# Optimization experiments

Hardware: AMD Instinct MI355X
Metric: run time of the kernel (lower is better)

The kernel has to match this reference:

```python
import jax, jax.numpy as jnp
import numpy as np

EMBED_SIZE = 768
HEAD_SIZE = 64
B, T = 4, 2048


def setup_inputs() -> dict:
    key = jax.random.key(0)
    kx, kk, kq, kv = jax.random.split(key, 4)
    x = jax.random.normal(kx, (B, T, EMBED_SIZE), dtype=jnp.float32)
    # torch Linear(E, H, bias=False): weight [H, E]; stored here as [E, H] for x @ W
    s = 1.0 / np.sqrt(EMBED_SIZE)
    Wk = jax.random.uniform(kk, (EMBED_SIZE, HEAD_SIZE), jnp.float32, -s, s)
    Wq = jax.random.uniform(kq, (EMBED_SIZE, HEAD_SIZE), jnp.float32, -s, s)
    Wv = jax.random.uniform(kv, (EMBED_SIZE, HEAD_SIZE), jnp.float32, -s, s)
    return {"x": x, "Wk": Wk, "Wq": Wq, "Wv": Wv}


def reference(x, Wk, Wq, Wv):
    Bx, Tx, E = x.shape
    k = x @ Wk  # [B, T, H]
    q = x @ Wq
    v = x @ Wv
    w = jnp.einsum("bth,bsh->bts", q, k)  # [B, T, T]
    causal = jnp.tril(jnp.ones((Tx, Tx), dtype=bool))
    # Faithful to source: mask to -inf FIRST, then scale by sqrt(embed_size)
    w = jnp.where(causal, w, -jnp.inf)
    w = w / jnp.sqrt(jnp.asarray(E, dtype=x.dtype))
    w = jax.nn.softmax(w, axis=-1)
    # dropout: eval mode / identity for the correctness baseline
    return jnp.einsum("bts,bsh->bth", w, v)
```

## Files before the change

kernel.cpp:

```cpp
#include <hip/hip_runtime.h>
#include <hip/hip_bf16.h>


typedef __attribute__((ext_vector_type(8))) short short8;
typedef __attribute__((ext_vector_type(4))) float f32x4;

#define SPLIT_KB 4
#define MAX_SP 8

__device__ __forceinline__ unsigned short f2bf(float f) {
    union { float f; unsigned u; } v; v.f = f;
    unsigned r = v.u + 0x7fffu + ((v.u >> 16) & 1u);
    return (unsigned short)(r >> 16);
}

__global__ __launch_bounds__(256) void proj_kernel(const float* __restrict__ x,
                                                   const float* __restrict__ Wk,
                                                   const float* __restrict__ Wq,
                                                   const float* __restrict__ Wv,
                                                   unsigned short* __restrict__ qws,
                                                   unsigned short* __restrict__ kws,
                                                   unsigned short* __restrict__ vT) {
    __shared__ unsigned short xs[32 * 72];
    __shared__ unsigned short wsm[64 * 72];
    const float CSCALE = 1.4426950408889634f / 27.712812921102035f;
    int tid = threadIdx.x;
    int lane = tid & 63, wave = tid >> 6;
    int quad = lane >> 4, l16 = lane & 15;
    int row0 = blockIdx.x * 32;
    int my = blockIdx.y;
    const float* W = (my == 0) ? Wq : (my == 1) ? Wk : Wv;

    int xrow = tid >> 3, xcb = (tid & 7) * 8;
    int wn = tid & 63, wk0 = (tid >> 6) * 16;

    f32x4 acc[2];
    acc[0] = (f32x4)(0.f); acc[1] = (f32x4)(0.f);

    for (int kc = 0; kc < 12; ++kc) {
        __syncthreads();
        {
            const float* src = x + (size_t)(row0 + xrow) * 768 + kc * 64 + xcb;
            float4 f0 = *(const float4*)(src);
            float4 f1 = *(const float4*)(src + 4);
            short8 pk;
            pk[0] = (short)f2bf(f0.x); pk[1] = (short)f2bf(f0.y);
            pk[2] = (short)f2bf(f0.z); pk[3] = (short)f2bf(f0.w);
            pk[4] = (short)f2bf(f1.x); pk[5] = (short)f2bf(f1.y);
            pk[6] = (short)f2bf(f1.z); pk[7] = (short)f2bf(f1.w);
            *(short8*)&xs[xrow * 72 + xcb] = pk;
        }
        {
            float wv[16];
            for (int i = 0; i < 16; ++i)
                wv[i] = W[(size_t)(kc * 64 + wk0 + i) * 64 + wn];
            if (my == 0)
                for (int i = 0; i < 16; ++i) wv[i] *= CSCALE;
            short8 p0, p1;
            for (int i = 0; i < 8; ++i) { p0[i] = (short)f2bf(wv[i]); p1[i] = (short)f2bf(wv[8 + i]); }
            *(short8*)&wsm[wn * 72 + wk0] = p0;
            *(short8*)&wsm[wn * 72 + wk0 + 8] = p1;
        }
        __syncthreads();
        for (int kh = 0; kh < 2; ++kh) {
            int kk = kh * 32 + quad * 8;
            short8 bfr = *(const short8*)&wsm[(wave * 16 + l16) * 72 + kk];
            for (int mt = 0; mt < 2; ++mt) {
                short8 a = *(const short8*)&xs[(mt * 16 + l16) * 72 + kk];
                acc[mt] = __builtin_amdgcn_mfma_f32_16x16x32_bf16(a, bfr, acc[mt], 0, 0, 0);
            }
        }
    }
    __syncthreads();
    int n = wave * 16 + l16;
    if (my != 2) {
        unsigned short* dst = (my == 0) ? qws : kws;
        for (int mt = 0; mt < 2; ++mt)
            for (int j = 0; j < 4; ++j) {
                int rloc = mt * 16 + quad * 4 + j;
                dst[(size_t)(row0 + rloc) * 64 + n] = f2bf(acc[mt][j]);
            }
    } else {
        for (int mt = 0; mt < 2; ++mt)
            for (int j = 0; j < 4; ++j) {
                int rloc = mt * 16 + quad * 4 + j;
                wsm[n * 40 + rloc] = f2bf(acc[mt][j]);
            }
        __syncthreads();
        int bidx = row0 >> 11, t0 = row0 & 2047;
        int c = tid >> 2, rb = (tid & 3) * 8;
        *(short8*)&vT[((size_t)(bidx * 64 + c)) * 2048 + t0 + rb] =
            *(const short8*)&wsm[c * 40 + rb];
    }
}

__global__ __launch_bounds__(128) void attn_split(const unsigned short* __restrict__ qws,
                                                  const unsigned short* __restrict__ kws,
                                                  const unsigned short* __restrict__ vT,
                                                  float* __restrict__ po,
                                                  float* __restrict__ pl,
                                                  float* __restrict__ out) {
    int bx = blockIdx.x, b = blockIdx.y, sp = blockIdx.z;
    int kbmax = (bx >> 1) + 1;
    int nsp = (kbmax + SPLIT_KB - 1) / SPLIT_KB;
    if (sp >= nsp) return;
    int kb_lo = sp * SPLIT_KB;
    int kb_hi = min(kb_lo + SPLIT_KB, kbmax);

    __shared__ unsigned short qs[32 * 72];
    __shared__ unsigned short ks[64 * 72];
    __shared__ unsigned short vs[64 * 72];
    __shared__ unsigned short ps[2][16 * 72];
    int tid = threadIdx.x;
    int lane = tid & 63, wave = tid >> 6;
    int quad = lane >> 4, l16 = lane & 15;
    int q0 = bx * 32;
    size_t qbase = ((size_t)b * 2048 + q0) * 64;
    for (int i = 0; i < 2; ++i) {
        int e = tid + 128 * i;
        int r = e >> 3, hb = (e & 7) * 8;
        *(short8*)&qs[r * 72 + hb] = *(const short8*)&qws[qbase + r * 64 + hb];
    }
    __syncthreads();
    short8 aq[2];
    for (int kh = 0; kh < 2; ++kh)
        aq[kh] = *(const short8*)&qs[(wave * 16 + l16) * 72 + kh * 32 + quad * 8];

    f32x4 o_acc[4];
    for (int nt = 0; nt < 4; ++nt) o_acc[nt] = (f32x4)(0.f);
    float l_run[4];
    int row_g[4];
    for (int j = 0; j < 4; ++j) {
        l_run[j] = 0.f;
        row_g[j] = q0 + wave * 16 + quad * 4 + j;
    }

    for (int kb = kb_lo; kb < kb_hi; ++kb) {
        __syncthreads();
        size_t kvbase = ((size_t)b * 2048 + kb * 64) * 64;
        for (int i = 0; i < 4; ++i) {
            int e = tid + 128 * i;
            int r = e >> 3, hb = (e & 7) * 8;
            *(short8*)&ks[r * 72 + hb] = *(const short8*)&kws[kvbase + r * 64 + hb];
        }
        for (int i = 0; i < 4; ++i) {
            int e = tid + 128 * i;
            int h = e >> 3, kyb = (e & 7) * 8;
            *(short8*)&vs[h * 72 + kyb] =
                *(const short8*)&vT[((size_t)b * 64 + h) * 2048 + kb * 64 + kyb];
        }
        __syncthreads();
        f32x4 s[4];
        for (int nt = 0; nt < 4; ++nt) s[nt] = (f32x4)(0.f);
        for (int kh = 0; kh < 2; ++kh)
            for (int nt = 0; nt < 4; ++nt) {
                short8 bk = *(const short8*)&ks[(nt * 16 + l16) * 72 + kh * 32 + quad * 8];
                s[nt] = __builtin_amdgcn_mfma_f32_16x16x32_bf16(aq[kh], bk, s[nt], 0, 0, 0);
            }
        if (kb == kbmax - 1) {
            for (int nt = 0; nt < 4; ++nt) {
                int key = kb * 64 + nt * 16 + l16;
                for (int j = 0; j < 4; ++j)
                    if (key > row_g[j]) s[nt][j] = -1e30f;
            }
        }
        for (int nt = 0; nt < 4; ++nt)
            for (int j = 0; j < 4; ++j) {
                float p = exp2f(s[nt][j]);
                l_run[j] += p;
                ps[wave][(quad * 4 + j) * 72 + nt * 16 + l16] = f2bf(p);
            }
        for (int kh = 0; kh < 2; ++kh) {
            short8 ap = *(const short8*)&ps[wave][l16 * 72 + kh * 32 + quad * 8];
            for (int nt = 0; nt < 4; ++nt) {
                short8 bv = *(const short8*)&vs[(nt * 16 + l16) * 72 + kh * 32 + quad * 8];
                o_acc[nt] = __builtin_amdgcn_mfma_f32_16x16x32_bf16(ap, bv, o_acc[nt], 0, 0, 0);
            }
        }
    }
    for (int off = 1; off < 16; off <<= 1)
        for (int j = 0; j < 4; ++j)
            l_run[j] += __shfl_xor(l_run[j], off, 16);

    if (nsp == 1) {
        for (int nt = 0; nt < 4; ++nt)
            for (int j = 0; j < 4; ++j)
                out[((size_t)b * 2048 + row_g[j]) * 64 + nt * 16 + l16] =
                    o_acc[nt][j] / l_run[j];
        return;
    }
    int sbase = ((b * 64 + bx) * MAX_SP + sp) * 32;
    for (int nt = 0; nt < 4; ++nt)
        for (int j = 0; j < 4; ++j) {
            int r = wave * 16 + quad * 4 + j;
            po[(size_t)(sbase + r) * 64 + nt * 16 + l16] = o_acc[nt][j];
        }
    if (l16 == 0) {
        for (int j = 0; j < 4; ++j) {
            int r = wave * 16 + quad * 4 + j;
            pl[sbase + r] = l_run[j];
        }
    }
}

__global__ __launch_bounds__(256) void reduce_kernel(const float* __restrict__ po,
                                                     const float* __restrict__ pl,
                                                     float* __restrict__ out) {
    int tid = threadIdx.x;
    int lane = tid & 63, wave = tid >> 6;
    int g = blockIdx.x * 4 + wave;
    int b = g >> 11, t = g & 2047;
    int bx = t >> 5, r = t & 31;
    int kbmax = (bx >> 1) + 1;
    int nsp = (kbmax + SPLIT_KB - 1) / SPLIT_KB;
    if (nsp == 1) return;
    int base = ((b * 64 + bx) * MAX_SP) * 32 + r;
    float acc = 0.f, lsum = 0.f;
    for (int sp = 0; sp < nsp; ++sp) {
        acc += po[(size_t)(base + sp * 32) * 64 + lane];
        lsum += pl[base + sp * 32];
    }
    out[(size_t)g * 64 + lane] = acc / lsum;
}

extern "C" void kernel_launch(void* const* d_in, const int* in_sizes, int n_in,
                              void* d_out, int out_size, void* d_ws, size_t ws_size,
                              hipStream_t stream) {
    const float* x  = (const float*)d_in[0];
    const float* Wk = (const float*)d_in[1];
    const float* Wq = (const float*)d_in[2];
    const float* Wv = (const float*)d_in[3];
    float* out = (float*)d_out;
    char* w = (char*)d_ws;
    unsigned short* qws = (unsigned short*)w;
    unsigned short* kws = (unsigned short*)(w + 1048576);
    unsigned short* vT  = (unsigned short*)(w + 2097152);
    float* po = (float*)(w + 3145728);
    float* pl = (float*)(w + 19922944);
    proj_kernel<<<dim3(256, 3), 256, 0, stream>>>(x, Wk, Wq, Wv, qws, kws, vT);
    attn_split<<<dim3(64, 4, MAX_SP), 128, 0, stream>>>(qws, kws, vT, po, pl, out);
    reduce_kernel<<<2048, 256, 0, stream>>>(po, pl, out);
}
```

Before: 101.6 us.

## Halve projection row tile and read weights directly into MFMA fragments

```diff
diff --git a/kernel.cpp b/kernel.cpp
--- a/kernel.cpp
+++ b/kernel.cpp
@@ -21,76 +21,63 @@
                                                    unsigned short* __restrict__ qws,
                                                    unsigned short* __restrict__ kws,
                                                    unsigned short* __restrict__ vT) {
-    __shared__ unsigned short xs[32 * 72];
-    __shared__ unsigned short wsm[64 * 72];
+    __shared__ unsigned short xs[16 * 72];
+    __shared__ unsigned short vsm[64 * 24];
     const float CSCALE = 1.4426950408889634f / 27.712812921102035f;
     int tid = threadIdx.x;
     int lane = tid & 63, wave = tid >> 6;
     int quad = lane >> 4, l16 = lane & 15;
-    int row0 = blockIdx.x * 32;
+    int row0 = blockIdx.x * 16;
     int my = blockIdx.y;
     const float* W = (my == 0) ? Wq : (my == 1) ? Wk : Wv;
 
-    int xrow = tid >> 3, xcb = (tid & 7) * 8;
-    int wn = tid & 63, wk0 = (tid >> 6) * 16;
-
-    f32x4 acc[2];
-    acc[0] = (f32x4)(0.f); acc[1] = (f32x4)(0.f);
+    int xrow = tid >> 4, xcb = (tid & 15) * 4;
+
+    f32x4 acc = (f32x4)(0.f);
 
     for (int kc = 0; kc < 12; ++kc) {
         __syncthreads();
         {
             const float* src = x + (size_t)(row0 + xrow) * 768 + kc * 64 + xcb;
             float4 f0 = *(const float4*)(src);
-            float4 f1 = *(const float4*)(src + 4);
-            short8 pk;
-            pk[0] = (short)f2bf(f0.x); pk[1] = (short)f2bf(f0.y);
-            pk[2] = (short)f2bf(f0.z); pk[3] = (short)f2bf(f0.w);
-            pk[4] = (short)f2bf(f1.x); pk[5] = (short)f2bf(f1.y);
-            pk[6] = (short)f2bf(f1.z); pk[7] = (short)f2bf(f1.w);
-            *(short8*)&xs[xrow * 72 + xcb] = pk;
-        }
-        {
-            float wv[16];
-            for (int i = 0; i < 16; ++i)
-                wv[i] = W[(size_t)(kc * 64 + wk0 + i) * 64 + wn];
-            if (my == 0)
-                for (int i = 0; i < 16; ++i) wv[i] *= CSCALE;
-            short8 p0, p1;
-            for (int i = 0; i < 8; ++i) { p0[i] = (short)f2bf(wv[i]); p1[i] = (short)f2bf(wv[8 + i]); }
-            *(short8*)&wsm[wn * 72 + wk0] = p0;
-            *(short8*)&wsm[wn * 72 + wk0 + 8] = p1;
+            unsigned short* d = &xs[xrow * 72 + xcb];
+            d[0] = f2bf(f0.x); d[1] = f2bf(f0.y);
+            d[2] = f2bf(f0.z); d[3] = f2bf(f0.w);
         }
         __syncthreads();
         for (int kh = 0; kh < 2; ++kh) {
-            int kk = kh * 32 + quad * 8;
-            short8 bfr = *(const short8*)&wsm[(wave * 16 + l16) * 72 + kk];
-            for (int mt = 0; mt < 2; ++mt) {
-                short8 a = *(const short8*)&xs[(mt * 16 + l16) * 72 + kk];
-                acc[mt] = __builtin_amdgcn_mfma_f32_16x16x32_bf16(a, bfr, acc[mt], 0, 0, 0);
-            }
-        }
-    }
-    __syncthreads();
+            short8 a = *(const short8*)&xs[l16 * 72 + kh * 32 + quad * 8];
+            const float* Wp = W + (size_t)(kc * 64 + kh * 32 + quad * 8) * 64
+                                + wave * 16 + l16;
+            short8 bfr;
+            #pragma unroll
+            for (int j = 0; j < 8; ++j) {
+                float wv = Wp[j * 64];
+                if (my == 0) wv *= CSCALE;
+                bfr[j] = (short)f2bf(wv);
+            }
+            acc = __builtin_amdgcn_mfma_f32_16x16x32_bf16(a, bfr, acc, 0, 0, 0);
+        }
+    }
     int n = wave * 16 + l16;
     if (my != 2) {
         unsigned short* dst = (my == 0) ? qws : kws;
-        for (int mt = 0; mt < 2; ++mt)
-            for (int j = 0; j < 4; ++j) {
-                int rloc = mt * 16 + quad * 4 + j;
-                dst[(size_t)(row0 + rloc) * 64 + n] = f2bf(acc[mt][j]);
-            }
+        for (int j = 0; j < 4; ++j) {
+            int rloc = quad * 4 + j;
+            dst[(size_t)(row0 + rloc) * 64 + n] = f2bf(acc[j]);
+        }
     } else {
-        for (int mt = 0; mt < 2; ++mt)
-            for (int j = 0; j < 4; ++j) {
-                int rloc = mt * 16 + quad * 4 + j;
-                wsm[n * 40 + rloc] = f2bf(acc[mt][j]);
-            }
-        __syncthreads();
-        int bidx = row0 >> 11, t0 = row0 & 2047;
-        int c = tid >> 2, rb = (tid & 3) * 8;
-        *(short8*)&vT[((size_t)(bidx * 64 + c)) * 2048 + t0 + rb] =
-            *(const short8*)&wsm[c * 40 + rb];
+        for (int j = 0; j < 4; ++j) {
+            int rloc = quad * 4 + j;
+            vsm[n * 24 + rloc] = f2bf(acc[j]);
+        }
+        __syncthreads();
+        if (tid < 128) {
+            int bidx = row0 >> 11, t0 = row0 & 2047;
+            int c = tid >> 1, rb = (tid & 1) * 8;
+            *(short8*)&vT[((size_t)(bidx * 64 + c)) * 2048 + t0 + rb] =
+                *(const short8*)&vsm[c * 24 + rb];
+        }
     }
 }
 
@@ -128,12 +115,10 @@
 
     f32x4 o_acc[4];
     for (int nt = 0; nt < 4; ++nt) o_acc[nt] = (f32x4)(0.f);
-    float l_run[4];
+    float l_run[4] = {0.f, 0.f, 0.f, 0.f};
     int row_g[4];
-    for (int j = 0; j < 4; ++j) {
-        l_run[j] = 0.f;
+    for (int j = 0; j < 4; ++j)
         row_g[j] = q0 + wave * 16 + quad * 4 + j;
-    }
 
     for (int kb = kb_lo; kb < kb_hi; ++kb) {
         __syncthreads();
@@ -237,7 +222,7 @@
     unsigned short* vT  = (unsigned short*)(w + 2097152);
     float* po = (float*)(w + 3145728);
     float* pl = (float*)(w + 19922944);
-    proj_kernel<<<dim3(256, 3), 256, 0, stream>>>(x, Wk, Wq, Wv, qws, kws, vT);
+    proj_kernel<<<dim3(512, 3), 256, 0, stream>>>(x, Wk, Wq, Wv, qws, kws, vT);
     attn_split<<<dim3(64, 4, MAX_SP), 128, 0, stream>>>(qws, kws, vT, po, pl, out);
     reduce_kernel<<<2048, 256, 0, stream>>>(po, pl, out);
 }
```

Result: slower. 109.4 us (+7.6%).

## Fuse projection, attention and reduction into one cooperative persistent kernel

Applied to the files above, without the earlier changes.

```diff
diff --git a/kernel.cpp b/kernel.cpp
--- a/kernel.cpp
+++ b/kernel.cpp
@@ -1,5 +1,8 @@
 #include <hip/hip_runtime.h>
 #include <hip/hip_bf16.h>
+#include <hip/hip_cooperative_groups.h>
+
+namespace cg = cooperative_groups;
 
 
 typedef __attribute__((ext_vector_type(8))) short short8;
@@ -12,6 +15,195 @@
     union { float f; unsigned u; } v; v.f = f;
     unsigned r = v.u + 0x7fffu + ((v.u >> 16) & 1u);
     return (unsigned short)(r >> 16);
+}
+
+__global__ __launch_bounds__(128, 2) void mega_kernel(
+        const float* __restrict__ x,  const float* __restrict__ Wk,
+        const float* __restrict__ Wq, const float* __restrict__ Wv,
+        unsigned short* __restrict__ qws, unsigned short* __restrict__ kws,
+        unsigned short* __restrict__ vT,  float* __restrict__ po,
+        float* __restrict__ pl, float* __restrict__ out) {
+    cg::grid_group grid = cg::this_grid();
+    __shared__ __align__(16) char smem[27648];
+    const float CSCALE = 1.4426950408889634f / 27.712812921102035f;
+    int tid = threadIdx.x;
+    int lane = tid & 63, wave = tid >> 6;
+    int quad = lane >> 4, l16 = lane & 15;
+
+    {
+        unsigned short* xs  = (unsigned short*)smem;
+        unsigned short* wsm = xs + 16 * 72;
+        unsigned short* vsm = wsm + 64 * 72;
+        int xrow = tid >> 3, xcb = (tid & 7) * 8;
+        int wn = tid & 63, wk0 = (tid >> 6) * 32;
+        for (int it = blockIdx.x; it < 1536; it += 512) {
+            int my = it >> 9;
+            int row0 = (it & 511) * 16;
+            const float* W = (my == 0) ? Wq : (my == 1) ? Wk : Wv;
+            f32x4 acc[2];
+            acc[0] = (f32x4)(0.f); acc[1] = (f32x4)(0.f);
+            for (int kc = 0; kc < 12; ++kc) {
+                __syncthreads();
+                {
+                    const float* src = x + (size_t)(row0 + xrow) * 768 + kc * 64 + xcb;
+                    float4 f0 = *(const float4*)(src);
+                    float4 f1 = *(const float4*)(src + 4);
+                    short8 pk;
+                    pk[0] = (short)f2bf(f0.x); pk[1] = (short)f2bf(f0.y);
+                    pk[2] = (short)f2bf(f0.z); pk[3] = (short)f2bf(f0.w);
+                    pk[4] = (short)f2bf(f1.x); pk[5] = (short)f2bf(f1.y);
+                    pk[6] = (short)f2bf(f1.z); pk[7] = (short)f2bf(f1.w);
+                    *(short8*)&xs[xrow * 72 + xcb] = pk;
+                }
+                for (int g = 0; g < 4; ++g) {
+                    float wv[8]; short8 p;
+                    #pragma unroll
+                    for (int i = 0; i < 8; ++i)
+                        wv[i] = W[(size_t)(kc * 64 + wk0 + g * 8 + i) * 64 + wn];
+                    if (my == 0)
+                        for (int i = 0; i < 8; ++i) wv[i] *= CSCALE;
+                    for (int i = 0; i < 8; ++i) p[i] = (short)f2bf(wv[i]);
+                    *(short8*)&wsm[wn * 72 + wk0 + g * 8] = p;
+                }
+                __syncthreads();
+                for (int kh = 0; kh < 2; ++kh) {
+                    int kk = kh * 32 + quad * 8;
+                    short8 a = *(const short8*)&xs[l16 * 72 + kk];
+                    for (int nt = 0; nt < 2; ++nt) {
+                        short8 bfr = *(const short8*)&wsm[(wave * 32 + nt * 16 + l16) * 72 + kk];
+                        acc[nt] = __builtin_amdgcn_mfma_f32_16x16x32_bf16(a, bfr, acc[nt], 0, 0, 0);
+                    }
+                }
+            }
+            if (my != 2) {
+                unsigned short* dst = (my == 0) ? qws : kws;
+                for (int nt = 0; nt < 2; ++nt)
+                    for (int j = 0; j < 4; ++j)
+                        dst[(size_t)(row0 + quad * 4 + j) * 64 + wave * 32 + nt * 16 + l16] =
+                            f2bf(acc[nt][j]);
+            } else {
+                for (int nt = 0; nt < 2; ++nt)
+                    for (int j = 0; j < 4; ++j)
+                        vsm[(wave * 32 + nt * 16 + l16) * 24 + quad * 4 + j] = f2bf(acc[nt][j]);
+                __syncthreads();
+                int bidx = row0 >> 11, t0 = row0 & 2047;
+                int c = tid >> 1, rb = (tid & 1) * 8;
+                *(short8*)&vT[((size_t)(bidx * 64 + c)) * 2048 + t0 + rb] =
+                    *(const short8*)&vsm[c * 24 + rb];
+            }
+        }
+    }
+    grid.sync();
+    {
+        unsigned short* qs = (unsigned short*)smem;
+        unsigned short* ks = qs + 32 * 72;
+        unsigned short* vs = ks + 64 * 72;
+        unsigned short* ps = vs + 64 * 72;
+        for (int i2 = blockIdx.x; i2 < 2048; i2 += 512) {
+            int bx = i2 & 63, b = (i2 >> 6) & 3, sp = i2 >> 8;
+            int kbmax = (bx >> 1) + 1;
+            int nsp = (kbmax + SPLIT_KB - 1) / SPLIT_KB;
+            if (sp >= nsp) continue;
+            int kb_lo = sp * SPLIT_KB;
+            int kb_hi = min(kb_lo + SPLIT_KB, kbmax);
+            int q0 = bx * 32;
+            size_t qbase = ((size_t)b * 2048 + q0) * 64;
+            for (int i = 0; i < 2; ++i) {
+                int e = tid + 128 * i;
+                int r = e >> 3, hb = (e & 7) * 8;
+                *(short8*)&qs[r * 72 + hb] = *(const short8*)&qws[qbase + r * 64 + hb];
+            }
+            __syncthreads();
+            short8 aq[2];
+            for (int kh = 0; kh < 2; ++kh)
+                aq[kh] = *(const short8*)&qs[(wave * 16 + l16) * 72 + kh * 32 + quad * 8];
+            f32x4 o_acc[4];
+            for (int nt = 0; nt < 4; ++nt) o_acc[nt] = (f32x4)(0.f);
+            float l_run[4] = {0.f, 0.f, 0.f, 0.f};
+            int row_g[4];
+            for (int j = 0; j < 4; ++j)
+                row_g[j] = q0 + wave * 16 + quad * 4 + j;
+            for (int kb = kb_lo; kb < kb_hi; ++kb) {
+                __syncthreads();
+                size_t kvbase = ((size_t)b * 2048 + kb * 64) * 64;
+                for (int i = 0; i < 4; ++i) {
+                    int e = tid + 128 * i;
+                    int r = e >> 3, hb = (e & 7) * 8;
+                    *(short8*)&ks[r * 72 + hb] = *(const short8*)&kws[kvbase + r * 64 + hb];
+                }
+                for (int i = 0; i < 4; ++i) {
+                    int e = tid + 128 * i;
+                    int h = e >> 3, kyb = (e & 7) * 8;
+                    *(short8*)&vs[h * 72 + kyb] =
+                        *(const short8*)&vT[((size_t)b * 64 + h) * 2048 + kb * 64 + kyb];
+                }
+                __syncthreads();
+                f32x4 s[4];
+                for (int nt = 0; nt < 4; ++nt) s[nt] = (f32x4)(0.f);
+                for (int kh = 0; kh < 2; ++kh)
+                    for (int nt = 0; nt < 4; ++nt) {
+                        short8 bk = *(const short8*)&ks[(nt * 16 + l16) * 72 + kh * 32 + quad * 8];
+                        s[nt] = __builtin_amdgcn_mfma_f32_16x16x32_bf16(aq[kh], bk, s[nt], 0, 0, 0);
+                    }
+                if (kb == kbmax - 1) {
+                    for (int nt = 0; nt < 4; ++nt) {
+                        int key = kb * 64 + nt * 16 + l16;
+                        for (int j = 0; j < 4; ++j)
+                            if (key > row_g[j]) s[nt][j] = -1e30f;
+                    }
+                }
+                for (int nt = 0; nt < 4; ++nt)
+                    for (int j = 0; j < 4; ++j) {
+                        float p = exp2f(s[nt][j]);
+                        l_run[j] += p;
+                        ps[wave * 1152 + (quad * 4 + j) * 72 + nt * 16 + l16] = f2bf(p);
+                    }
+                for (int kh = 0; kh < 2; ++kh) {
+                    short8 ap = *(const short8*)&ps[wave * 1152 + l16 * 72 + kh * 32 + quad * 8];
+                    for (int nt = 0; nt < 4; ++nt) {
+                        short8 bv = *(const short8*)&vs[(nt * 16 + l16) * 72 + kh * 32 + quad * 8];
+                        o_acc[nt] = __builtin_amdgcn_mfma_f32_16x16x32_bf16(ap, bv, o_acc[nt], 0, 0, 0);
+                    }
+                }
+            }
+            for (int off = 1; off < 16; off <<= 1)
+                for (int j = 0; j < 4; ++j)
+                    l_run[j] += __shfl_xor(l_run[j], off, 16);
+            if (nsp == 1) {
+                for (int nt = 0; nt < 4; ++nt)
+                    for (int j = 0; j < 4; ++j)
+                        out[((size_t)b * 2048 + row_g[j]) * 64 + nt * 16 + l16] =
+                            o_acc[nt][j] / l_run[j];
+                continue;
+            }
+            int sbase = ((b * 64 + bx) * MAX_SP + sp) * 32;
+            for (int nt = 0; nt < 4; ++nt)
+                for (int j = 0; j < 4; ++j) {
+                    int r = wave * 16 + quad * 4 + j;
+                    po[(size_t)(sbase + r) * 64 + nt * 16 + l16] = o_acc[nt][j];
+                }
+            if (l16 == 0)
+                for (int j = 0; j < 4; ++j) {
+                    int r = wave * 16 + quad * 4 + j;
+                    pl[sbase + r] = l_run[j];
+                }
+        }
+    }
+    grid.sync();
+    for (int g = blockIdx.x * 2 + wave; g < 8192; g += 1024) {
+        int b = g >> 11, t = g & 2047;
+        int bx = t >> 5, r = t & 31;
+        int kbmax = (bx >> 1) + 1;
+        int nsp = (kbmax + SPLIT_KB - 1) / SPLIT_KB;
+        if (nsp == 1) continue;
+        int base = ((b * 64 + bx) * MAX_SP) * 32 + r;
+        float acc = 0.f, lsum = 0.f;
+        for (int sp = 0; sp < nsp; ++sp) {
+            acc += po[(size_t)(base + sp * 32) * 64 + lane];
+            lsum += pl[base + sp * 32];
+        }
+        out[(size_t)g * 64 + lane] = acc / lsum;
+    }
 }
 
 __global__ __launch_bounds__(256) void proj_kernel(const float* __restrict__ x,
@@ -30,13 +222,10 @@
     int row0 = blockIdx.x * 32;
     int my = blockIdx.y;
     const float* W = (my == 0) ? Wq : (my == 1) ? Wk : Wv;
-
     int xrow = tid >> 3, xcb = (tid & 7) * 8;
     int wn = tid & 63, wk0 = (tid >> 6) * 16;
-
     f32x4 acc[2];
     acc[0] = (f32x4)(0.f); acc[1] = (f32x4)(0.f);
-
     for (int kc = 0; kc < 12; ++kc) {
         __syncthreads();
         {
@@ -106,7 +295,6 @@
     if (sp >= nsp) return;
     int kb_lo = sp * SPLIT_KB;
     int kb_hi = min(kb_lo + SPLIT_KB, kbmax);
-
     __shared__ unsigned short qs[32 * 72];
     __shared__ unsigned short ks[64 * 72];
     __shared__ unsigned short vs[64 * 72];
@@ -125,16 +313,12 @@
     short8 aq[2];
     for (int kh = 0; kh < 2; ++kh)
         aq[kh] = *(const short8*)&qs[(wave * 16 + l16) * 72 + kh * 32 + quad * 8];
-
     f32x4 o_acc[4];
     for (int nt = 0; nt < 4; ++nt) o_acc[nt] = (f32x4)(0.f);
-    float l_run[4];
+    float l_run[4] = {0.f, 0.f, 0.f, 0.f};
     int row_g[4];
-    for (int j = 0; j < 4; ++j) {
-        l_run[j] = 0.f;
+    for (int j = 0; j < 4; ++j)
         row_g[j] = q0 + wave * 16 + quad * 4 + j;
-    }
-
     for (int kb = kb_lo; kb < kb_hi; ++kb) {
         __syncthreads();
         size_t kvbase = ((size_t)b * 2048 + kb * 64) * 64;
@@ -181,7 +365,6 @@
     for (int off = 1; off < 16; off <<= 1)
         for (int j = 0; j < 4; ++j)
             l_run[j] += __shfl_xor(l_run[j], off, 16);
-
     if (nsp == 1) {
         for (int nt = 0; nt < 4; ++nt)
             for (int j = 0; j < 4; ++j)
@@ -195,12 +378,11 @@
             int r = wave * 16 + quad * 4 + j;
             po[(size_t)(sbase + r) * 64 + nt * 16 + l16] = o_acc[nt][j];
         }
-    if (l16 == 0) {
+    if (l16 == 0)
         for (int j = 0; j < 4; ++j) {
             int r = wave * 16 + quad * 4 + j;
             pl[sbase + r] = l_run[j];
         }
-    }
 }
 
 __global__ __launch_bounds__(256) void reduce_kernel(const float* __restrict__ po,
@@ -237,7 +419,15 @@
     unsigned short* vT  = (unsigned short*)(w + 2097152);
     float* po = (float*)(w + 3145728);
     float* pl = (float*)(w + 19922944);
-    proj_kernel<<<dim3(256, 3), 256, 0, stream>>>(x, Wk, Wq, Wv, qws, kws, vT);
-    attn_split<<<dim3(64, 4, MAX_SP), 128, 0, stream>>>(qws, kws, vT, po, pl, out);
-    reduce_kernel<<<2048, 256, 0, stream>>>(po, pl, out);
-}
+    void* args[] = {(void*)&x, (void*)&Wk, (void*)&Wq, (void*)&Wv,
+                    (void*)&qws, (void*)&kws, (void*)&vT,
+                    (void*)&po, (void*)&pl, (void*)&out};
+    hipError_t err = hipLaunchCooperativeKernel((void*)mega_kernel, dim3(512),
+                                                dim3(128), args, 0, stream);
+    if (err != hipSuccess) {
+        (void)hipGetLastError();
+        proj_kernel<<<dim3(256, 3), 256, 0, stream>>>(x, Wk, Wq, Wv, qws, kws, vT);
+        attn_split<<<dim3(64, 4, MAX_SP), 128, 0, stream>>>(qws, kws, vT, po, pl, out);
+        reduce_kernel<<<2048, 256, 0, stream>>>(po, pl, out);
+    }
+}
```

Measured after the change: 280.6 us. 2.76x slower.
